# Kernel tuning notes

Hardware: AMD Instinct MI355X
Metric: run time of the kernel (lower is better)

Reference implementation:

```python
import jax, jax.numpy as jnp
import numpy as np
from jax import lax

T, B, D, H = 512, 2048, 64, 10  # time, batch, input_dim, hidden_dim (= n_qubits)
CLIP = 5.0


def setup_inputs() -> dict:
    key = jax.random.key(0)
    ks = jax.random.split(key, 5)
    inputs = jax.random.normal(ks[0], (T, B, D), jnp.float32)

    def lin(k):
        kw, kb = jax.random.split(k)
        W = jax.random.normal(kw, (H, D + H), jnp.float32) * 0.1
        b = jax.random.normal(kb, (H,), jnp.float32) * 0.1
        return W, b

    Wf, bf = lin(ks[1])
    Wi, bi = lin(ks[2])
    Wu, bu = lin(ks[3])
    Wo, bo = lin(ks[4])
    return dict(inputs=inputs, Wf=Wf, bf=bf, Wi=Wi, bi=bi,
                Wu=Wu, bu=bu, Wo=Wo, bo=bo)


def _quantum_gate(p):
    # Analytic statevector result: RX(p_q) per qubit then CX chain q->q+1.
    # <Z_q> = prod_{j<=q} cos(p_j); Qiskit big-endian labels reverse the order.
    return jnp.flip(jnp.cumprod(jnp.cos(p), axis=-1), axis=-1)


def _fcl(hx):
    # RY(hx_q) per qubit, measure Z on qubit n-1 (label 'Z'+'I'*(n-1)) -> cos(hx[:, -1])
    return jnp.cos(hx[:, -1:])  # [B, 1]


def reference(inputs, Wf, bf, Wi, bi, Wu, bu, Wo, bo):
    Bsz = inputs.shape[1]
    Hd = Wf.shape[0]
    h0 = jnp.zeros((Bsz, Hd), inputs.dtype)
    c0 = jnp.zeros((Bsz, Hd), inputs.dtype)

    def step(carry, x):
        hx, cx = carry
        comb = jnp.concatenate([x, hx], axis=1)  # [B, D+H]
        clip = lambda z: jnp.clip(z, -CLIP, CLIP)
        f = jax.nn.sigmoid(_quantum_gate(clip(comb @ Wf.T + bf)))
        i = jax.nn.sigmoid(_quantum_gate(clip(comb @ Wi.T + bi)))
        g = jnp.tanh(_quantum_gate(clip(comb @ Wu.T + bu)))
        o = jax.nn.sigmoid(_quantum_gate(clip(comb @ Wo.T + bo)))
        cx = f * cx + i * g
        hx = o * jnp.tanh(cx)
        hx = hx * _fcl(hx)  # scalar modulation broadcast over hidden dim
        return (hx, cx), hx

    (hx, cx), outputs = lax.scan(step, (h0, c0), inputs)
    return outputs, (hx, cx)
```

## Files before the change

kernel.cpp:

```cpp
#include <hip/hip_runtime.h>

#define TT    512
#define BATCH 2048
#define DIN   64
#define HD    10
#define WROW  (DIN + HD)

__global__ __launch_bounds__(64, 2)
void qlstm_kernel(const float* __restrict__ X,
                  const float* __restrict__ Wf, const float* __restrict__ bf,
                  const float* __restrict__ Wi, const float* __restrict__ bi,
                  const float* __restrict__ Wu, const float* __restrict__ bu,
                  const float* __restrict__ Wo, const float* __restrict__ bo,
                  float* __restrict__ out)
{
    const int row  = blockIdx.x;
    const int lane = threadIdx.x;
    const int g    = lane >> 4;
    const int v    = lane & 15;
    const bool act_lane = (v >= 6);

    __shared__ float xs[2][DIN];

    const float LOG2E  = 1.4426950408889634f;
    const float INV2PI = 0.15915494309189535f;

    float cmul = -LOG2E, amul = 1.f, aadd = 0.f;
    const float* Wg = Wf; const float* bg = bf;
    if (g == 1) { Wg = Wi; bg = bi; }
    else if (g == 2) { Wg = Wu; bg = bu; cmul = -2.f * LOG2E; amul = 2.f; aadd = -1.f; }
    else if (g == 3) { Wg = Wo; bg = bo; }

    float wx[DIN];
    float wh[HD];
    float bias = 0.f;
    if (act_lane) {
        const int uw = 15 - v;
        #pragma unroll
        for (int k = 0; k < DIN; ++k) wx[k] = Wg[uw * WROW + k];
        #pragma unroll
        for (int k = 0; k < HD; ++k)  wh[k] = Wg[uw * WROW + DIN + k];
        bias = bg[uw];
    } else {
        #pragma unroll
        for (int k = 0; k < DIN; ++k) wx[k] = 0.f;
        #pragma unroll
        for (int k = 0; k < HD; ++k)  wh[k] = 0.f;
    }

    float h[HD];
    #pragma unroll
    for (int k = 0; k < HD; ++k) h[k] = 0.f;
    float c = 0.f;
    float hkeep = 0.f;

    const size_t xstep = (size_t)BATCH * DIN;
    const size_t xbase = (size_t)row * DIN + lane;

    xs[0][lane] = X[xbase];
    float xr = X[xstep + xbase];

    float zx;
    {
        float s0 = bias, s1 = 0.f, s2 = 0.f, s3 = 0.f;
        #pragma unroll
        for (int k = 0; k < DIN; k += 4) {
            float4 xq = *reinterpret_cast<const float4*>(&xs[0][k]);
            s0 = fmaf(wx[k + 0], xq.x, s0);
            s1 = fmaf(wx[k + 1], xq.y, s1);
            s2 = fmaf(wx[k + 2], xq.z, s2);
            s3 = fmaf(wx[k + 3], xq.w, s3);
        }
        zx = (s0 + s1) + (s2 + s3);
    }

    int cur = 0;
    for (int t = 0; t < TT; ++t) {
        const int nxt = cur ^ 1;
        if (t + 1 < TT) xs[nxt][lane] = xr;
        if (t + 2 < TT) xr = X[(size_t)(t + 2) * xstep + xbase];

        float za = zx, zb = 0.f;
        #pragma unroll
        for (int j = 0; j < HD; j += 2) {
            za = fmaf(wh[j],     h[j],     za);
            zb = fmaf(wh[j + 1], h[j + 1], zb);
        }
        float z = za + zb;
        z = fminf(fmaxf(z, -5.f), 5.f);
        float p = __builtin_amdgcn_cosf(z * INV2PI);

        {
            int s_;
            s_ = __builtin_amdgcn_update_dpp(0x3f800000, __float_as_int(p), 0x101, 0xF, 0xF, false);
            p *= __int_as_float(s_);
            s_ = __builtin_amdgcn_update_dpp(0x3f800000, __float_as_int(p), 0x102, 0xF, 0xF, false);
            p *= __int_as_float(s_);
            s_ = __builtin_amdgcn_update_dpp(0x3f800000, __float_as_int(p), 0x104, 0xF, 0xF, false);
            p *= __int_as_float(s_);
            s_ = __builtin_amdgcn_update_dpp(0x3f800000, __float_as_int(p), 0x108, 0xF, 0xF, false);
            p *= __int_as_float(s_);
        }

        float e = __builtin_amdgcn_exp2f(cmul * p);
        float a = amul * __builtin_amdgcn_rcpf(1.f + e) + aadd;

        float fg = __shfl(a, v);
        float ig = __shfl(a, 16 + v);
        float ug = __shfl(a, 32 + v);
        float og = __shfl(a, 48 + v);

        c = fmaf(fg, c, ig * ug);
        float e2 = __builtin_amdgcn_exp2f(-2.f * LOG2E * c);
        float th = 2.f * __builtin_amdgcn_rcpf(1.f + e2) - 1.f;
        float hpre = og * th;
        float h9 = __int_as_float(__builtin_amdgcn_readlane(__float_as_int(hpre), 15));
        float m  = __builtin_amdgcn_cosf(h9 * INV2PI);
        float hnew = hpre * m;
        hkeep = hnew;

        if (lane >= 6 && lane < 16) out[((size_t)t * BATCH + row) * HD + (lane - 6)] = hnew;

        #pragma unroll
        for (int j = 0; j < HD; ++j)
            h[j] = __int_as_float(__builtin_amdgcn_readlane(__float_as_int(hnew), 6 + j));

        if (t + 1 < TT) {
            float s0 = bias, s1 = 0.f, s2 = 0.f, s3 = 0.f;
            const float* xp = xs[nxt];
            #pragma unroll
            for (int k = 0; k < DIN; k += 4) {
                float4 xq = *reinterpret_cast<const float4*>(&xp[k]);
                s0 = fmaf(wx[k + 0], xq.x, s0);
                s1 = fmaf(wx[k + 1], xq.y, s1);
                s2 = fmaf(wx[k + 2], xq.z, s2);
                s3 = fmaf(wx[k + 3], xq.w, s3);
            }
            zx = (s0 + s1) + (s2 + s3);
        }
        cur = nxt;
    }

    if (lane >= 6 && lane < 16) {
        const size_t base = (size_t)TT * BATCH * HD;
        out[base + (size_t)row * HD + (lane - 6)] = hkeep;
        out[base + (size_t)BATCH * HD + (size_t)row * HD + (lane - 6)] = c;
    }
}

extern "C" void kernel_launch(void* const* d_in, const int* in_sizes, int n_in,
                              void* d_out, int out_size, void* d_ws, size_t ws_size,
                              hipStream_t stream) {
    const float* X  = (const float*)d_in[0];
    const float* Wf = (const float*)d_in[1];
    const float* bf = (const float*)d_in[2];
    const float* Wi = (const float*)d_in[3];
    const float* bi = (const float*)d_in[4];
    const float* Wu = (const float*)d_in[5];
    const float* bu = (const float*)d_in[6];
    const float* Wo = (const float*)d_in[7];
    const float* bo = (const float*)d_in[8];
    float* out = (float*)d_out;

    qlstm_kernel<<<BATCH, 64, 0, stream>>>(X, Wf, bf, Wi, bi, Wu, bu, Wo, bo, out);
}
```

Before: 638.5 us.

## Precompute input projections in a separate GEMM kernel before recurrence

Splits the work into two kernels. A parallel kernel first computes the input projection X·Wx^T + b for every timestep into a workspace buffer. A recurrence kernel then only reads those precomputed values, prefetched three steps ahead, and does the small hidden-state matvec plus the gate math. This takes the 64-wide input dot product off the serial per-step critical path, at the cost of writing and re-reading a roughly 170MB workspace. If the workspace is too small, it falls back to the original fused kernel.

```diff
diff --git a/kernel.cpp b/kernel.cpp
--- a/kernel.cpp
+++ b/kernel.cpp
@@ -5,14 +5,180 @@
 #define DIN   64
 #define HD    10
 #define WROW  (DIN + HD)
-
-__global__ __launch_bounds__(64, 2)
-void qlstm_kernel(const float* __restrict__ X,
+#define NGATE 40
+#define ZSTRIDE (BATCH * NGATE)
+#define ZNEED ((size_t)(TT + 4) * ZSTRIDE * 4)
+
+__global__ __launch_bounds__(256, 2)
+void zgemm_kernel(const float* __restrict__ X,
                   const float* __restrict__ Wf, const float* __restrict__ bf,
                   const float* __restrict__ Wi, const float* __restrict__ bi,
                   const float* __restrict__ Wu, const float* __restrict__ bu,
                   const float* __restrict__ Wo, const float* __restrict__ bo,
-                  float* __restrict__ out)
+                  float* __restrict__ Z)
+{
+    const int tid  = threadIdx.x;
+    const int n    = tid & 63;
+    const int msub = tid >> 6;
+    __shared__ float xs[16][64];
+
+    float w[DIN];
+    float bias = 0.f;
+    {
+        const float* Wg = Wf; const float* bg = bf;
+        const int g = n / HD;
+        if (g == 1) { Wg = Wi; bg = bi; }
+        else if (g == 2) { Wg = Wu; bg = bu; }
+        else if (g == 3) { Wg = Wo; bg = bo; }
+        const int q = n - g * HD;
+        if (n < NGATE) {
+            #pragma unroll
+            for (int k = 0; k < DIN; ++k) w[k] = Wg[q * WROW + k];
+            bias = bg[q];
+        } else {
+            #pragma unroll
+            for (int k = 0; k < DIN; ++k) w[k] = 0.f;
+        }
+    }
+
+    const size_t m0 = (size_t)blockIdx.x * 64;
+    #pragma unroll 1
+    for (int c = 0; c < 4; ++c) {
+        const size_t mc = m0 + (size_t)c * 16;
+        __syncthreads();
+        {
+            const float4 xv = *reinterpret_cast<const float4*>(&X[mc * DIN + (size_t)tid * 4]);
+            *reinterpret_cast<float4*>(&xs[0][0] + tid * 4) = xv;
+        }
+        __syncthreads();
+        #pragma unroll
+        for (int j = 0; j < 4; ++j) {
+            const int ml = msub * 4 + j;
+            float s0 = bias, s1 = 0.f, s2 = 0.f, s3 = 0.f;
+            #pragma unroll
+            for (int k = 0; k < DIN; k += 4) {
+                float4 xq = *reinterpret_cast<const float4*>(&xs[ml][k]);
+                s0 = fmaf(w[k + 0], xq.x, s0);
+                s1 = fmaf(w[k + 1], xq.y, s1);
+                s2 = fmaf(w[k + 2], xq.z, s2);
+                s3 = fmaf(w[k + 3], xq.w, s3);
+            }
+            if (n < NGATE) Z[(mc + ml) * NGATE + n] = (s0 + s1) + (s2 + s3);
+        }
+    }
+}
+
+__global__ __launch_bounds__(64, 2)
+void qlstm_rec_kernel(const float* __restrict__ Z,
+                      const float* __restrict__ Wf, const float* __restrict__ Wi,
+                      const float* __restrict__ Wu, const float* __restrict__ Wo,
+                      float* __restrict__ out)
+{
+    const int row  = blockIdx.x;
+    const int lane = threadIdx.x;
+    const int g    = lane >> 4;
+    const int v    = lane & 15;
+    const bool act_lane = (v >= 6);
+
+    const float LOG2E  = 1.4426950408889634f;
+    const float INV2PI = 0.15915494309189535f;
+
+    float cmul = -LOG2E, amul = 1.f, aadd = 0.f;
+    const float* Wg = Wf;
+    if (g == 1) { Wg = Wi; }
+    else if (g == 2) { Wg = Wu; cmul = -2.f * LOG2E; amul = 2.f; aadd = -1.f; }
+    else if (g == 3) { Wg = Wo; }
+
+    float wh[HD];
+    if (act_lane) {
+        const int uw = 15 - v;
+        #pragma unroll
+        for (int k = 0; k < HD; ++k) wh[k] = Wg[uw * WROW + DIN + k];
+    } else {
+        #pragma unroll
+        for (int k = 0; k < HD; ++k) wh[k] = 0.f;
+    }
+
+    int n = g * HD + (15 - v);
+    if (n > NGATE - 1) n = NGATE - 1;
+    const float* Zp = Z + (size_t)row * NGATE + n;
+
+    float h[HD];
+    #pragma unroll
+    for (int k = 0; k < HD; ++k) h[k] = 0.f;
+    float c = 0.f;
+    float hkeep = 0.f;
+
+    float z0 = Zp[0];
+    float z1 = Zp[(size_t)ZSTRIDE];
+    float z2 = Zp[(size_t)2 * ZSTRIDE];
+
+    #pragma unroll 1
+    for (int t = 0; t < TT; ++t) {
+        const float zx = z0;
+        z0 = z1; z1 = z2;
+        z2 = Zp[(size_t)(t + 3) * ZSTRIDE];
+
+        float za = zx, zb = 0.f;
+        #pragma unroll
+        for (int j = 0; j < HD; j += 2) {
+            za = fmaf(wh[j],     h[j],     za);
+            zb = fmaf(wh[j + 1], h[j + 1], zb);
+        }
+        float z = za + zb;
+        z = fminf(fmaxf(z, -5.f), 5.f);
+        float p = __builtin_amdgcn_cosf(z * INV2PI);
+
+        {
+            int s_;
+            s_ = __builtin_amdgcn_update_dpp(0x3f800000, __float_as_int(p), 0x101, 0xF, 0xF, false);
+            p *= __int_as_float(s_);
+            s_ = __builtin_amdgcn_update_dpp(0x3f800000, __float_as_int(p), 0x102, 0xF, 0xF, false);
+            p *= __int_as_float(s_);
+            s_ = __builtin_amdgcn_update_dpp(0x3f800000, __float_as_int(p), 0x104, 0xF, 0xF, false);
+            p *= __int_as_float(s_);
+            s_ = __builtin_amdgcn_update_dpp(0x3f800000, __float_as_int(p), 0x108, 0xF, 0xF, false);
+            p *= __int_as_float(s_);
+        }
+
+        float e = __builtin_amdgcn_exp2f(cmul * p);
+        float a = amul * __builtin_amdgcn_rcpf(1.f + e) + aadd;
+
+        float fg = __shfl(a, v);
+        float ig = __shfl(a, 16 + v);
+        float ug = __shfl(a, 32 + v);
+        float og = __shfl(a, 48 + v);
+
+        c = fmaf(fg, c, ig * ug);
+        float e2 = __builtin_amdgcn_exp2f(-2.f * LOG2E * c);
+        float th = 2.f * __builtin_amdgcn_rcpf(1.f + e2) - 1.f;
+        float hpre = og * th;
+        float h9 = __int_as_float(__builtin_amdgcn_readlane(__float_as_int(hpre), 15));
+        float m  = __builtin_amdgcn_cosf(h9 * INV2PI);
+        float hnew = hpre * m;
+        hkeep = hnew;
+
+        if (lane >= 6 && lane < 16) out[((size_t)t * BATCH + row) * HD + (lane - 6)] = hnew;
+
+        #pragma unroll
+        for (int j = 0; j < HD; ++j)
+            h[j] = __int_as_float(__builtin_amdgcn_readlane(__float_as_int(hnew), 6 + j));
+    }
+
+    if (lane >= 6 && lane < 16) {
+        const size_t base = (size_t)TT * BATCH * HD;
+        out[base + (size_t)row * HD + (lane - 6)] = hkeep;
+        out[base + (size_t)BATCH * HD + (size_t)row * HD + (lane - 6)] = c;
+    }
+}
+
+__global__ __launch_bounds__(64, 2)
+void qlstm_fused_kernel(const float* __restrict__ X,
+                        const float* __restrict__ Wf, const float* __restrict__ bf,
+                        const float* __restrict__ Wi, const float* __restrict__ bi,
+                        const float* __restrict__ Wu, const float* __restrict__ bu,
+                        const float* __restrict__ Wo, const float* __restrict__ bo,
+                        float* __restrict__ out)
 {
     const int row  = blockIdx.x;
     const int lane = threadIdx.x;
@@ -162,5 +328,13 @@
     const float* bo = (const float*)d_in[8];
     float* out = (float*)d_out;
 
-    qlstm_kernel<<<BATCH, 64, 0, stream>>>(X, Wf, bf, Wi, bi, Wu, bu, Wo, bo, out);
+    if (ws_size >= ZNEED) {
+        float* Zbuf = (float*)d_ws;
+        zgemm_kernel<<<(TT * BATCH) / 64, 256, 0, stream>>>(
+            X, Wf, bf, Wi, bi, Wu, bu, Wo, bo, Zbuf);
+        qlstm_rec_kernel<<<BATCH, 64, 0, stream>>>(Zbuf, Wf, Wi, Wu, Wo, out);
+    } else {
+        qlstm_fused_kernel<<<BATCH, 64, 0, stream>>>(
+            X, Wf, bf, Wi, bi, Wu, bu, Wo, bo, out);
+    }
 }
```

Result: slower. 711.6 us (+11.4%).
